# Performance work log

Hardware: AMD Instinct MI355X
Metric: run time of the kernel (lower is better)

The kernel has to match this reference:

```python
import jax, jax.numpy as jnp
import numpy as np

N_NODES = 100000
N_EDGES = 3200000
BATCH = 16
LAYER_NUMBER = 4


def setup_inputs() -> dict:
    key = jax.random.key(0)
    k1, k2, k3, k4 = jax.random.split(key, 4)
    x = jax.random.normal(k1, (N_NODES, BATCH), dtype=jnp.float32)
    # learnable per-edge weights (log1p(counts) at init in the original; the
    # parameter itself is what is learned, so a plain random init is faithful)
    weights = jax.random.normal(k2, (N_EDGES,), dtype=jnp.float32)
    row = jax.random.randint(k3, (N_EDGES,), 0, N_NODES, dtype=jnp.int64)
    col = jax.random.randint(k4, (N_EDGES,), 0, N_NODES, dtype=jnp.int64)
    return {"x": x, "weights": weights, "row": row, "col": col}


def reference(x, weights, row, col):
    # Repeated sparse COO SpMM: y <- A @ y, applied layer_number times,
    # where A[row[e], col[e]] = weights[e].
    def step(y, _):
        msg = weights[:, None] * y[col]                      # [E, B] gather + scale
        y_new = jax.ops.segment_sum(msg, row, num_segments=N_NODES)  # [N, B] scatter-add
        return y_new, None

    y, _ = jax.lax.scan(step, x, None, length=LAYER_NUMBER)
    return y
```

## Files before the change

kernel.cpp:

```cpp
#include <hip/hip_runtime.h>

#define N_NODES 100000
#define N_EDGES 3200000
#define BATCH 16
#define BKT_SHIFT 6
#define BKT_NODES 64
#define K_BUCKETS 1563
#define NB 128
#define FT 512
#define CHUNK (N_EDGES / NB)
#define SCAN_T 256
#define SCAN_C 7
#define CAP 4096

__global__ void hist_kernel(const int* __restrict__ row, int* __restrict__ blk_cnt) {
    __shared__ int lh[K_BUCKETS];
    int t = threadIdx.x, blk = blockIdx.x;
    for (int k = t; k < K_BUCKETS; k += FT) lh[k] = 0;
    __syncthreads();
    int base = blk * CHUNK;
    for (int e = base + t; e < base + CHUNK; e += FT)
        atomicAdd(&lh[row[e] >> BKT_SHIFT], 1);
    __syncthreads();
    for (int k = t; k < K_BUCKETS; k += FT)
        blk_cnt[k * NB + blk] = lh[k];
}

__global__ void colscan_kernel(int* __restrict__ blk_cnt, int* __restrict__ totals) {
    int bkt = blockIdx.x * blockDim.x + threadIdx.x;
    if (bkt >= K_BUCKETS) return;
    int4* p = (int4*)&blk_cnt[bkt * NB];
    int acc = 0;
    for (int q = 0; q < NB / 4; q++) {
        int4 v = p[q];
        int4 o;
        o.x = acc; acc += v.x;
        o.y = acc; acc += v.y;
        o.z = acc; acc += v.z;
        o.w = acc; acc += v.w;
        p[q] = o;
    }
    totals[bkt] = acc;
}

__global__ void scan_kernel(const int* __restrict__ totals, int* __restrict__ bptr,
                            int* __restrict__ row_ptr) {
    __shared__ int s[SCAN_T];
    int t = threadIdx.x;
    int loc[SCAN_C];
    int sum = 0;
    for (int i = 0; i < SCAN_C; i++) {
        int idx = t * SCAN_C + i;
        int v = (idx < K_BUCKETS) ? totals[idx] : 0;
        loc[i] = v;
        sum += v;
    }
    s[t] = sum;
    __syncthreads();
    for (int off = 1; off < SCAN_T; off <<= 1) {
        int x = (t >= off) ? s[t - off] : 0;
        __syncthreads();
        s[t] += x;
        __syncthreads();
    }
    int excl = s[t] - sum;
    for (int i = 0; i < SCAN_C; i++) {
        int idx = t * SCAN_C + i;
        if (idx < K_BUCKETS) bptr[idx] = excl;
        excl += loc[i];
    }
    if (t == 0) { bptr[K_BUCKETS] = N_EDGES; row_ptr[N_NODES] = N_EDGES; }
}

__global__ void fill_kernel(const int* __restrict__ row, const int* __restrict__ col,
                            const float* __restrict__ w,
                            const int* __restrict__ bptr, const int* __restrict__ blk_cnt,
                            uint2* __restrict__ entries) {
    __shared__ int lbase[K_BUCKETS];
    __shared__ int lcur[K_BUCKETS];
    int t = threadIdx.x, blk = blockIdx.x;
    for (int k = t; k < K_BUCKETS; k += FT) {
        lbase[k] = bptr[k] + blk_cnt[k * NB + blk];
        lcur[k] = 0;
    }
    __syncthreads();
    int base = blk * CHUNK;
    for (int e = base + t; e < base + CHUNK; e += FT) {
        int r = row[e];
        int bkt = r >> BKT_SHIFT;
        int loc = atomicAdd(&lcur[bkt], 1);
        entries[lbase[bkt] + loc] =
            make_uint2(((unsigned)(r & (BKT_NODES - 1)) << 17) | (unsigned)col[e],
                       __float_as_uint(w[e]));
    }
}

__global__ void nodesort_kernel(const int* __restrict__ bptr, uint2* __restrict__ entries,
                                int* __restrict__ row_ptr) {
    __shared__ uint2 ebuf[CAP];
    __shared__ int nh[BKT_NODES];
    __shared__ int nc[BKT_NODES];
    int t = threadIdx.x, b = blockIdx.x;
    int beg = bptr[b], end = bptr[b + 1];
    int n = min(end - beg, CAP);
    if (t < BKT_NODES) nh[t] = 0;
    __syncthreads();
    for (int k = t; k < n; k += 256) {
        uint2 r = entries[beg + k];
        ebuf[k] = r;
        atomicAdd(&nh[r.x >> 17], 1);
    }
    __syncthreads();
    if (t == 0) {
        int acc = 0;
        for (int i = 0; i < BKT_NODES; i++) {
            int v = nh[i];
            int node = b * BKT_NODES + i;
            if (node < N_NODES) row_ptr[node] = beg + acc;
            nc[i] = acc;
            acc += v;
        }
    }
    __syncthreads();
    for (int k = t; k < n; k += 256) {
        uint2 r = ebuf[k];
        int pos = atomicAdd(&nc[r.x >> 17], 1);
        entries[beg + pos] = r;
    }
}

__global__ void __launch_bounds__(256) pull_kernel(const float* __restrict__ y,
                            const uint2* __restrict__ entries,
                            const int* __restrict__ row_ptr,
                            float* __restrict__ out) {
    int tid = blockIdx.x * blockDim.x + threadIdx.x;
    int node = tid >> 4;
    int b = tid & 15;
    if (node >= N_NODES) return;
    int beg = row_ptr[node];
    int end = row_ptr[node + 1];
    float acc = 0.f;
    if (beg < end) {
        int lim = end - 1;
        uint2 r[8];
        #pragma unroll
        for (int j = 0; j < 8; j++) r[j] = entries[min(beg + j, lim)];
        int i = beg;
        while (i + 8 <= end) {
            float yv[8];
            #pragma unroll
            for (int j = 0; j < 8; j++)
                yv[j] = y[(r[j].x & 0x1FFFFu) * BATCH + b];
            uint2 nx[8];
            #pragma unroll
            for (int j = 0; j < 8; j++)
                nx[j] = entries[min(i + 8 + j, lim)];
            #pragma unroll
            for (int j = 0; j < 8; j++)
                acc += __uint_as_float(r[j].y) * yv[j];
            #pragma unroll
            for (int j = 0; j < 8; j++) r[j] = nx[j];
            i += 8;
        }
        if (i < end) {
            float yv[8];
            #pragma unroll
            for (int j = 0; j < 8; j++)
                yv[j] = y[(r[j].x & 0x1FFFFu) * BATCH + b];
            #pragma unroll
            for (int j = 0; j < 8; j++)
                if (i + j < end)
                    acc += __uint_as_float(r[j].y) * yv[j];
        }
    }
    out[node * BATCH + b] = acc;
}

extern "C" void kernel_launch(void* const* d_in, const int* in_sizes, int n_in,
                              void* d_out, int out_size, void* d_ws, size_t ws_size,
                              hipStream_t stream) {
    const float* x   = (const float*)d_in[0];
    const float* w   = (const float*)d_in[1];
    const int*   row = (const int*)d_in[2];
    const int*   col = (const int*)d_in[3];
    float*       out = (float*)d_out;

    char* p = (char*)d_ws;
    uint2* entries = (uint2*)p;  p += (size_t)N_EDGES * sizeof(uint2);
    float* buf     = (float*)p;
    int*   blk_cnt = (int*)buf;
    p += (size_t)N_NODES * BATCH * sizeof(float);
    int* totals  = (int*)p;      p += 8192;
    int* bptr    = (int*)p;      p += 8192;
    int* row_ptr = (int*)p;

    hist_kernel<<<NB, FT, 0, stream>>>(row, blk_cnt);
    colscan_kernel<<<(K_BUCKETS + 255) / 256, 256, 0, stream>>>(blk_cnt, totals);
    scan_kernel<<<1, SCAN_T, 0, stream>>>(totals, bptr, row_ptr);
    fill_kernel<<<NB, FT, 0, stream>>>(row, col, w, bptr, blk_cnt, entries);
    nodesort_kernel<<<K_BUCKETS, 256, 0, stream>>>(bptr, entries, row_ptr);

    const int pgrid = (N_NODES * BATCH + 255) / 256;
    pull_kernel<<<pgrid, 256, 0, stream>>>(x,   entries, row_ptr, buf);
    pull_kernel<<<pgrid, 256, 0, stream>>>(buf, entries, row_ptr, out);
    pull_kernel<<<pgrid, 256, 0, stream>>>(out, entries, row_ptr, buf);
    pull_kernel<<<pgrid, 256, 0, stream>>>(buf, entries, row_ptr, out);
}
```

Before: 363.8 us.

## Stage bucketed COO entries in LDS for coalesced per-bucket global writes

The fill kernel now builds a local histogram and exclusive scan per block, then scatters entries into a shared-memory buffer grouped by bucket. Eight lanes per bucket then copy each contiguous run to its global position, replacing scattered single 8-byte global writes. The block count is doubled to 256, so each block's chunk (about 100KB of entries) fits in LDS. The histogram kernel drops to 256 threads. This costs a second pass over row, a 512-wide in-block scan, and heavy LDS use that limits occupancy to one block per CU.

After: 362.5 us. About the same (-0.4%).

```diff
diff --git a/kernel.cpp b/kernel.cpp
--- a/kernel.cpp
+++ b/kernel.cpp
@@ -6,9 +6,9 @@
 #define BKT_SHIFT 6
 #define BKT_NODES 64
 #define K_BUCKETS 1563
-#define NB 128
+#define NB 256
+#define SUB (N_EDGES / NB)
 #define FT 512
-#define CHUNK (N_EDGES / NB)
 #define SCAN_T 256
 #define SCAN_C 7
 #define CAP 4096
@@ -16,13 +16,13 @@
 __global__ void hist_kernel(const int* __restrict__ row, int* __restrict__ blk_cnt) {
     __shared__ int lh[K_BUCKETS];
     int t = threadIdx.x, blk = blockIdx.x;
-    for (int k = t; k < K_BUCKETS; k += FT) lh[k] = 0;
-    __syncthreads();
-    int base = blk * CHUNK;
-    for (int e = base + t; e < base + CHUNK; e += FT)
+    for (int k = t; k < K_BUCKETS; k += 256) lh[k] = 0;
+    __syncthreads();
+    int base = blk * SUB;
+    for (int e = base + t; e < base + SUB; e += 256)
         atomicAdd(&lh[row[e] >> BKT_SHIFT], 1);
     __syncthreads();
-    for (int k = t; k < K_BUCKETS; k += FT)
+    for (int k = t; k < K_BUCKETS; k += 256)
         blk_cnt[k * NB + blk] = lh[k];
 }
 
@@ -72,26 +72,62 @@
     if (t == 0) { bptr[K_BUCKETS] = N_EDGES; row_ptr[N_NODES] = N_EDGES; }
 }
 
-__global__ void fill_kernel(const int* __restrict__ row, const int* __restrict__ col,
-                            const float* __restrict__ w,
-                            const int* __restrict__ bptr, const int* __restrict__ blk_cnt,
-                            uint2* __restrict__ entries) {
-    __shared__ int lbase[K_BUCKETS];
+__global__ void __launch_bounds__(FT) fill_kernel(
+        const int* __restrict__ row, const int* __restrict__ col,
+        const float* __restrict__ w,
+        const int* __restrict__ bptr, const int* __restrict__ blk_cnt,
+        uint2* __restrict__ entries) {
+    __shared__ uint2 sbuf[SUB];
+    __shared__ int lbeg[K_BUCKETS];
     __shared__ int lcur[K_BUCKETS];
+    __shared__ int sscan[FT];
     int t = threadIdx.x, blk = blockIdx.x;
-    for (int k = t; k < K_BUCKETS; k += FT) {
-        lbase[k] = bptr[k] + blk_cnt[k * NB + blk];
-        lcur[k] = 0;
-    }
-    __syncthreads();
-    int base = blk * CHUNK;
-    for (int e = base + t; e < base + CHUNK; e += FT) {
+    for (int k = t; k < K_BUCKETS; k += FT) lcur[k] = 0;
+    __syncthreads();
+    int base = blk * SUB;
+    for (int e = base + t; e < base + SUB; e += FT)
+        atomicAdd(&lcur[row[e] >> BKT_SHIFT], 1);
+    __syncthreads();
+    int loc[4];
+    int sum = 0;
+    #pragma unroll
+    for (int j = 0; j < 4; j++) {
+        int k = t * 4 + j;
+        int v = (k < K_BUCKETS) ? lcur[k] : 0;
+        loc[j] = v;
+        sum += v;
+    }
+    sscan[t] = sum;
+    __syncthreads();
+    for (int off = 1; off < FT; off <<= 1) {
+        int x = (t >= off) ? sscan[t - off] : 0;
+        __syncthreads();
+        sscan[t] += x;
+        __syncthreads();
+    }
+    int excl = sscan[t] - sum;
+    #pragma unroll
+    for (int j = 0; j < 4; j++) {
+        int k = t * 4 + j;
+        if (k < K_BUCKETS) { lbeg[k] = excl; lcur[k] = excl; }
+        excl += loc[j];
+    }
+    __syncthreads();
+    for (int e = base + t; e < base + SUB; e += FT) {
         int r = row[e];
         int bkt = r >> BKT_SHIFT;
-        int loc = atomicAdd(&lcur[bkt], 1);
-        entries[lbase[bkt] + loc] =
-            make_uint2(((unsigned)(r & (BKT_NODES - 1)) << 17) | (unsigned)col[e],
-                       __float_as_uint(w[e]));
+        int pos = atomicAdd(&lcur[bkt], 1);
+        sbuf[pos] = make_uint2(((unsigned)(r & (BKT_NODES - 1)) << 17) | (unsigned)col[e],
+                               __float_as_uint(w[e]));
+    }
+    __syncthreads();
+    int lane = t & 7;
+    for (int k = (t >> 3); k < K_BUCKETS; k += FT / 8) {
+        int lb = lbeg[k];
+        int le = lcur[k];
+        int dst = bptr[k] + blk_cnt[k * NB + blk];
+        for (int i = lb + lane; i < le; i += 8)
+            entries[dst + (i - lb)] = sbuf[i];
     }
 }
 
@@ -194,7 +230,7 @@
     int* bptr    = (int*)p;      p += 8192;
     int* row_ptr = (int*)p;
 
-    hist_kernel<<<NB, FT, 0, stream>>>(row, blk_cnt);
+    hist_kernel<<<NB, 256, 0, stream>>>(row, blk_cnt);
     colscan_kernel<<<(K_BUCKETS + 255) / 256, 256, 0, stream>>>(blk_cnt, totals);
     scan_kernel<<<1, SCAN_T, 0, stream>>>(totals, bptr, row_ptr);
     fill_kernel<<<NB, FT, 0, stream>>>(row, col, w, bptr, blk_cnt, entries);
```
